# Performance work log

Measured on AMD Instinct MI355X. Metric: run time of the kernel, lower is better.

Reference implementation:

```python
import jax, jax.numpy as jnp
import numpy as np


def setup_inputs() -> dict:
    key = jax.random.key(0)
    ks = jax.random.split(key, 5)
    T, B, I, H = 512, 32, 1024, 1024
    # W/U are the stacked [W_i;W_f;W_c;W_o] and [U_i;U_f;U_c;U_o] gate weights (i,f,c,o order)
    x = jax.random.normal(ks[0], (T, B, I), dtype=jnp.float32)
    W = jax.random.normal(ks[1], (4 * H, I), dtype=jnp.float32) * (1.0 / np.sqrt(I))
    U = jax.random.normal(ks[2], (4 * H, H), dtype=jnp.float32) * (1.0 / np.sqrt(H))
    bias_ih = jax.random.normal(ks[3], (4 * H,), dtype=jnp.float32) * 0.1
    bias_hh = jax.random.normal(ks[4], (4 * H,), dtype=jnp.float32) * 0.1
    return {"x": x, "W": W, "U": U, "bias_ih": bias_ih, "bias_hh": bias_hh}


def reference(x, W, U, bias_ih, bias_hh):
    # RecurrentDropoutLSTMCell with dropout=0 (masks == 1.0), unidirectional, 1 layer.
    T, B, I = x.shape
    H = U.shape[1]
    # Precompute all input-side gate projections in one big GEMM: [T,B,4H]
    xg = jnp.einsum('tbi,gi->tbg', x, W) + (bias_ih + bias_hh)

    def step(carry, xg_t):
        h, c = carry
        g = xg_t + h @ U.T  # [B,4H]
        i_t = jax.nn.sigmoid(g[:, :H])
        f_t = jax.nn.sigmoid(g[:, H:2 * H])
        c_hat = jnp.tanh(g[:, 2 * H:3 * H])
        o_t = jax.nn.sigmoid(g[:, 3 * H:])
        c_t = f_t * c + i_t * c_hat
        h_t = o_t * jnp.tanh(c_t)
        return (h_t, c_t), h_t

    h0 = jnp.zeros((B, H), dtype=x.dtype)
    c0 = jnp.zeros((B, H), dtype=x.dtype)
    (h_n, c_n), output = jax.lax.scan(step, (h0, c0), xg)
    # matches torch module: output [T,B,H], next_hidden = (h_n,c_n) each [1,B,H]
    return output, h_n[None], c_n[None]
```

## Files before the change

### kernel.cpp

```cpp
#include <hip/hip_runtime.h>
#include <hip/hip_bf16.h>
#include <cstdint>
#include <cstddef>

#define TSTEPS 512
#define BATCH  32
#define HDIM   1024
#define GDIM   4096
#define NBLK   64

typedef __attribute__((ext_vector_type(8))) short short8;
typedef __attribute__((ext_vector_type(4))) float f32x4;

__device__ __forceinline__ unsigned short f2bf(float f) {
  uint32_t u = __float_as_uint(f);
  uint32_t r = (u + 0x7FFFu + ((u >> 16) & 1u)) >> 16;
  return (unsigned short)r;
}

__device__ __forceinline__ void async_ld16(const void* gptr, void* ldsptr) {
  __builtin_amdgcn_global_load_lds(
      (const __attribute__((address_space(1))) void*)gptr,
      (__attribute__((address_space(3))) void*)ldsptr, 16, 0, 0);
}

__global__ void cvt_bf16(const float* __restrict__ s, unsigned short* __restrict__ d, int n4) {
  int i = blockIdx.x * blockDim.x + threadIdx.x;
  if (i < n4) {
    float4 v = ((const float4*)s)[i];
    ushort4 o;
    o.x = f2bf(v.x); o.y = f2bf(v.y); o.z = f2bf(v.z); o.w = f2bf(v.w);
    ((ushort4*)d)[i] = o;
  }
}

__global__ void reorder_U(const float* __restrict__ U, unsigned short* __restrict__ Ur) {
  int i = blockIdx.x * blockDim.x + threadIdx.x;
  if (i >= GDIM * (HDIM / 4)) return;
  int k4 = i & 255;
  int row_o = i >> 8;
  int blk = row_o >> 6;
  int rem = row_o & 63;
  int g = rem >> 4;
  int jj = rem & 15;
  int src_row = g * HDIM + blk * 16 + jj;
  float4 v = ((const float4*)(U + (size_t)src_row * HDIM))[k4];
  ushort4 o;
  o.x = f2bf(v.x); o.y = f2bf(v.y); o.z = f2bf(v.z); o.w = f2bf(v.w);
  ((ushort4*)(Ur + (size_t)row_o * HDIM))[k4] = o;
}

__global__ void __launch_bounds__(256) gemm_xg(
    const unsigned short* __restrict__ A, const unsigned short* __restrict__ Bw,
    const float* __restrict__ bias_ih, const float* __restrict__ bias_hh,
    float* __restrict__ C) {
  __shared__ unsigned short As[128 * 32];
  __shared__ unsigned short Bs[128 * 32];
  const int tid = threadIdx.x;
  const int lane = tid & 63;
  const int wave = tid >> 6;
  const int m0 = blockIdx.x * 128;
  const int n0 = blockIdx.y * 128;
  const int wy = wave >> 1, wx = wave & 1;

  f32x4 acc[4][4] = {};
  const int srow = lane >> 2;
  const int skoff = (lane & 3) * 8;

  for (int k0 = 0; k0 < 1024; k0 += 32) {
    for (int s = 0; s < 2; ++s) {
      int ch = wave * 2 + s;
      int row = ch * 16 + srow;
      async_ld16(A + (size_t)(m0 + row) * 1024 + k0 + skoff, (char*)As + ch * 1024);
      async_ld16(Bw + (size_t)(n0 + row) * 1024 + k0 + skoff, (char*)Bs + ch * 1024);
    }
    __syncthreads();

    const int fr = lane & 15;
    const int fo = (lane >> 4) * 8;
    short8 a[4], b[4];
#pragma unroll
    for (int i = 0; i < 4; ++i)
      a[i] = *(const short8*)(As + (wy * 64 + i * 16 + fr) * 32 + fo);
#pragma unroll
    for (int j = 0; j < 4; ++j)
      b[j] = *(const short8*)(Bs + (wx * 64 + j * 16 + fr) * 32 + fo);
#pragma unroll
    for (int i = 0; i < 4; ++i)
#pragma unroll
      for (int j = 0; j < 4; ++j)
        acc[i][j] = __builtin_amdgcn_mfma_f32_16x16x32_bf16(a[i], b[j], acc[i][j], 0, 0, 0);
    __syncthreads();
  }

  const int fr = lane & 15;
  const int rq = (lane >> 4) * 4;
#pragma unroll
  for (int j = 0; j < 4; ++j) {
    int n = n0 + wx * 64 + j * 16 + fr;
    float bsum = bias_ih[n] + bias_hh[n];
#pragma unroll
    for (int i = 0; i < 4; ++i) {
      int mbase = m0 + wy * 64 + i * 16 + rq;
#pragma unroll
      for (int rr = 0; rr < 4; ++rr)
        C[(size_t)(mbase + rr) * GDIM + n] = acc[i][j][rr] + bsum;
    }
  }
}

__global__ void init_state(unsigned short* __restrict__ h0, float* __restrict__ c0,
                           unsigned int* __restrict__ flags) {
  int i = blockIdx.x * blockDim.x + threadIdx.x;
  if (i < 2 * BATCH * HDIM) h0[i] = 0;
  if (i < BATCH * HDIM) c0[i] = 0.f;
  if (i < NBLK * 32) flags[i] = 0;
}

__global__ void __launch_bounds__(256, 1) lstm_persist(
    const float* __restrict__ xg,
    const unsigned short* __restrict__ Urp,
    unsigned short* __restrict__ hbuf,
    float* __restrict__ cbuf,
    float* __restrict__ out,
    unsigned int* __restrict__ flags,
    int t0, int Tc) {
  __shared__ float partials[4][64][33];
  __shared__ float ex[32][17];
  const int tid = threadIdx.x;
  const int lane = tid & 63;
  const int wave = tid >> 6;
  const int blk = blockIdx.x;

  short8 Af[4][8];
  {
    const int ar = lane & 15;
    const int ak = (lane >> 4) * 8;
#pragma unroll
    for (int mt = 0; mt < 4; ++mt) {
      const unsigned short* base =
          Urp + (size_t)(blk * 64 + mt * 16 + ar) * 1024 + wave * 256 + ak;
#pragma unroll
      for (int s = 0; s < 8; ++s) Af[mt][s] = *(const short8*)(base + s * 32);
    }
  }

  const int b = tid & 31;
  const int jjb = tid >> 5;
  float creg0 = cbuf[b * 1024 + blk * 16 + jjb];
  float creg1 = cbuf[b * 1024 + blk * 16 + jjb + 8];

  float xgv[8];
  auto ld_xg = [&](int tl) {
    const float* p = xg + ((size_t)tl * 32 + b) * GDIM + blk * 16 + jjb;
#pragma unroll
    for (int g = 0; g < 4; ++g) {
      xgv[g * 2 + 0] = p[g * 1024];
      xgv[g * 2 + 1] = p[g * 1024 + 8];
    }
  };
  ld_xg(0);

  for (int tl = 0; tl < Tc; ++tl) {
    const int t = t0 + tl;
    const unsigned short* hprev = hbuf + (size_t)(t & 1) * (BATCH * HDIM);
    unsigned short* hnext = hbuf + (size_t)((t + 1) & 1) * (BATCH * HDIM);

    short8 Bf[2][8];
    {
      const int kb = wave * 256 + (lane >> 4) * 8;
#pragma unroll
      for (int nt = 0; nt < 2; ++nt) {
        const unsigned short* hb = hprev + (size_t)(nt * 16 + (lane & 15)) * 1024 + kb;
#pragma unroll
        for (int s = 0; s < 8; ++s) Bf[nt][s] = *(const short8*)(hb + s * 32);
      }
    }

    f32x4 acc[4][2] = {};
#pragma unroll
    for (int s = 0; s < 8; ++s)
#pragma unroll
      for (int mt = 0; mt < 4; ++mt)
#pragma unroll
        for (int nt = 0; nt < 2; ++nt)
          acc[mt][nt] =
              __builtin_amdgcn_mfma_f32_16x16x32_bf16(Af[mt][s], Bf[nt][s], acc[mt][nt], 0, 0, 0);

    {
      const int q4 = (lane >> 4) * 4;
      const int cc = lane & 15;
#pragma unroll
      for (int mt = 0; mt < 4; ++mt)
#pragma unroll
        for (int nt = 0; nt < 2; ++nt)
#pragma unroll
          for (int r = 0; r < 4; ++r)
            partials[wave][mt * 16 + q4 + r][nt * 16 + cc] = acc[mt][nt][r];
    }
    __syncthreads();

    float hv0, hv1;
#pragma unroll
    for (int h2 = 0; h2 < 2; ++h2) {
      const int jj = jjb + 8 * h2;
      float g[4];
#pragma unroll
      for (int gate = 0; gate < 4; ++gate) {
        const int row = gate * 16 + jj;
        g[gate] = partials[0][row][b] + partials[1][row][b] + partials[2][row][b] +
                  partials[3][row][b] + xgv[gate * 2 + h2];
      }
      float it = 1.f / (1.f + __expf(-g[0]));
      float ft = 1.f / (1.f + __expf(-g[1]));
      float ch = tanhf(g[2]);
      float ot = 1.f / (1.f + __expf(-g[3]));
      float& cr = h2 ? creg1 : creg0;
      cr = ft * cr + it * ch;
      float hvv = ot * tanhf(cr);
      if (h2) hv1 = hvv; else hv0 = hvv;
    }
    ex[b][jjb] = hv0;
    ex[b][jjb + 8] = hv1;
    __syncthreads();

    const int b2 = tid >> 3;
    const int pr = tid & 7;
    const float v0 = ex[b2][pr * 2];
    const float v1 = ex[b2][pr * 2 + 1];
    const size_t off = (size_t)b2 * 1024 + blk * 16 + pr * 2;
    {
      unsigned int pk = (unsigned)f2bf(v0) | ((unsigned)f2bf(v1) << 16);
      __hip_atomic_store((unsigned int*)(hnext + off), pk, __ATOMIC_RELAXED,
                         __HIP_MEMORY_SCOPE_AGENT);
    }

    const bool not_last = (tl + 1 < Tc);

    if (not_last) {
      asm volatile("s_waitcnt vmcnt(0)" ::: "memory");
      __syncthreads();
      if (tid == 0)
        __hip_atomic_store(&flags[blk * 32], (unsigned)(t + 1), __ATOMIC_RELAXED,
                           __HIP_MEMORY_SCOPE_AGENT);
    }

    {
      *(float2*)(out + (size_t)t * (BATCH * HDIM) + off) = make_float2(v0, v1);
      if (t == TSTEPS - 1)
        *(float2*)(out + (size_t)TSTEPS * (BATCH * HDIM) + off) = make_float2(v0, v1);
    }

    if (not_last) {
      ld_xg(tl + 1);
      if (wave == 0) {
        while (__hip_atomic_load(&flags[lane * 32], __ATOMIC_RELAXED,
                                 __HIP_MEMORY_SCOPE_AGENT) < (unsigned)(t + 1)) {
        }
        __builtin_amdgcn_fence(__ATOMIC_ACQUIRE, "agent");
      }
      __syncthreads();
    }
  }

  cbuf[b * 1024 + blk * 16 + jjb] = creg0;
  cbuf[b * 1024 + blk * 16 + jjb + 8] = creg1;
  if (t0 + Tc == TSTEPS) {
    float* cn = out + (size_t)TSTEPS * (BATCH * HDIM) + (BATCH * HDIM);
    cn[b * 1024 + blk * 16 + jjb] = creg0;
    cn[b * 1024 + blk * 16 + jjb + 8] = creg1;
  }
}

extern "C" void kernel_launch(void* const* d_in, const int* in_sizes, int n_in,
                              void* d_out, int out_size, void* d_ws, size_t ws_size,
                              hipStream_t stream) {
  const float* x = (const float*)d_in[0];
  const float* W = (const float*)d_in[1];
  const float* U = (const float*)d_in[2];
  const float* b_ih = (const float*)d_in[3];
  const float* b_hh = (const float*)d_in[4];
  float* out = (float*)d_out;

  char* ws = (char*)d_ws;
  const size_t MB8 = (size_t)8 << 20;
  unsigned short* Wb = (unsigned short*)ws;
  unsigned short* Urp = (unsigned short*)(ws + MB8);
  unsigned short* hbuf = (unsigned short*)(ws + 2 * MB8);
  float* cbuf = (float*)(ws + 2 * MB8 + 131072);
  unsigned int* flags = (unsigned int*)(ws + 2 * MB8 + 262144);
  char* chunkbase = ws + 2 * MB8 + 262144 + 16384;

  const size_t fixed_bytes = 2 * MB8 + 262144 + 16384;
  const size_t per_t = (size_t)BATCH * GDIM * 4 + (size_t)BATCH * HDIM * 2;
  int Tc = TSTEPS;
  while (Tc > 8 && fixed_bytes + (size_t)Tc * per_t > ws_size) Tc >>= 1;

  unsigned short* xb = (unsigned short*)chunkbase;
  float* xg = (float*)(chunkbase + (size_t)Tc * BATCH * HDIM * 2);

  cvt_bf16<<<4096, 256, 0, stream>>>(W, Wb, GDIM * HDIM / 4);
  reorder_U<<<4096, 256, 0, stream>>>(U, Urp);
  init_state<<<256, 256, 0, stream>>>(hbuf, cbuf, flags);

  for (int c0 = 0; c0 < TSTEPS; c0 += Tc) {
    const int Mc = Tc * BATCH;
    cvt_bf16<<<(Mc * HDIM / 4 + 255) / 256, 256, 0, stream>>>(
        x + (size_t)c0 * BATCH * HDIM, xb, Mc * HDIM / 4);
    gemm_xg<<<dim3(Mc / 128, GDIM / 128), 256, 0, stream>>>(xb, Wb, b_ih, b_hh, xg);

    const float* xg_arg = xg;
    const unsigned short* urp_arg = Urp;
    unsigned short* hbuf_arg = hbuf;
    float* cbuf_arg = cbuf;
    float* out_arg = out;
    unsigned int* flags_arg = flags;
    int t0_arg = c0, tc_arg = Tc;
    void* args[] = {&xg_arg, &urp_arg, &hbuf_arg, &cbuf_arg,
                    &out_arg, &flags_arg, &t0_arg, &tc_arg};
    hipLaunchCooperativeKernel((void*)lstm_persist, dim3(NBLK), dim3(256), args, 0, stream);
  }
}
```

Baseline: 3.121 ms.

## Split each LSTM timestep into two batch halves with finer-grained cross-block flags

The persistent LSTM kernel now processes each timestep as two 16-batch halves, each with its own MFMA pass, gate epilogue, h store and flag post. Blocks wait per half-step, so a block can begin the second half's matmul while others are still finishing theirs. This pipelines across the grid barrier instead of serializing a full 32-batch step. It doubles the number of flag waits and syncthreads per step and adds a spin-limit break that could silently continue without synchronization if exceeded.

```diff
diff --git a/kernel.cpp b/kernel.cpp
--- a/kernel.cpp
+++ b/kernel.cpp
@@ -8,6 +8,7 @@
 #define HDIM   1024
 #define GDIM   4096
 #define NBLK   64
+#define SPIN_LIMIT (1u << 22)
 
 typedef __attribute__((ext_vector_type(8))) short short8;
 typedef __attribute__((ext_vector_type(4))) float f32x4;
@@ -125,8 +126,8 @@
     float* __restrict__ out,
     unsigned int* __restrict__ flags,
     int t0, int Tc) {
-  __shared__ float partials[4][64][33];
-  __shared__ float ex[32][17];
+  __shared__ float partials[4][64][17];
+  __shared__ float ex[16][17];
   const int tid = threadIdx.x;
   const int lane = tid & 63;
   const int wave = tid >> 6;
@@ -145,130 +146,126 @@
     }
   }
 
-  const int b = tid & 31;
-  const int jjb = tid >> 5;
-  float creg0 = cbuf[b * 1024 + blk * 16 + jjb];
-  float creg1 = cbuf[b * 1024 + blk * 16 + jjb + 8];
-
-  float xgv[8];
-  auto ld_xg = [&](int tl) {
-    const float* p = xg + ((size_t)tl * 32 + b) * GDIM + blk * 16 + jjb;
-#pragma unroll
-    for (int g = 0; g < 4; ++g) {
-      xgv[g * 2 + 0] = p[g * 1024];
-      xgv[g * 2 + 1] = p[g * 1024 + 8];
-    }
+  const int b_loc = tid & 15;
+  const int jj = tid >> 4;
+  float creg[2];
+  creg[0] = cbuf[(b_loc) * 1024 + blk * 16 + jj];
+  creg[1] = cbuf[(16 + b_loc) * 1024 + blk * 16 + jj];
+
+  float xgv[4];
+  auto ld_xg = [&](int tl_, int hb_) {
+    const float* p = xg + ((size_t)tl_ * 32 + hb_ * 16 + b_loc) * GDIM + blk * 16 + jj;
+#pragma unroll
+    for (int g = 0; g < 4; ++g) xgv[g] = p[g * 1024];
   };
-  ld_xg(0);
+  ld_xg(0, 0);
 
   for (int tl = 0; tl < Tc; ++tl) {
-    const int t = t0 + tl;
-    const unsigned short* hprev = hbuf + (size_t)(t & 1) * (BATCH * HDIM);
-    unsigned short* hnext = hbuf + (size_t)((t + 1) & 1) * (BATCH * HDIM);
-
-    short8 Bf[2][8];
-    {
-      const int kb = wave * 256 + (lane >> 4) * 8;
-#pragma unroll
-      for (int nt = 0; nt < 2; ++nt) {
-        const unsigned short* hb = hprev + (size_t)(nt * 16 + (lane & 15)) * 1024 + kb;
-#pragma unroll
-        for (int s = 0; s < 8; ++s) Bf[nt][s] = *(const short8*)(hb + s * 32);
-      }
-    }
-
-    f32x4 acc[4][2] = {};
-#pragma unroll
-    for (int s = 0; s < 8; ++s)
-#pragma unroll
-      for (int mt = 0; mt < 4; ++mt)
-#pragma unroll
-        for (int nt = 0; nt < 2; ++nt)
-          acc[mt][nt] =
-              __builtin_amdgcn_mfma_f32_16x16x32_bf16(Af[mt][s], Bf[nt][s], acc[mt][nt], 0, 0, 0);
-
-    {
-      const int q4 = (lane >> 4) * 4;
-      const int cc = lane & 15;
-#pragma unroll
-      for (int mt = 0; mt < 4; ++mt)
-#pragma unroll
-        for (int nt = 0; nt < 2; ++nt)
+#pragma unroll
+    for (int hb = 0; hb < 2; ++hb) {
+      const int t = t0 + tl;
+      const unsigned short* hprev = hbuf + (size_t)(t & 1) * (BATCH * HDIM);
+      unsigned short* hnext = hbuf + (size_t)((t + 1) & 1) * (BATCH * HDIM);
+
+      if (tl > 0) {
+        if (wave == 0) {
+          const unsigned target = (unsigned)(2 * t + hb - 1);
+          unsigned spins = 0;
+          while (__hip_atomic_load(&flags[lane * 32], __ATOMIC_RELAXED,
+                                   __HIP_MEMORY_SCOPE_AGENT) < target) {
+            if (++spins > SPIN_LIMIT) break;
+          }
+          __builtin_amdgcn_fence(__ATOMIC_ACQUIRE, "agent");
+        }
+        __syncthreads();
+      }
+
+      short8 Bf[8];
+      {
+        const int kb = wave * 256 + (lane >> 4) * 8;
+        const unsigned short* hbp =
+            hprev + (size_t)(hb * 16 + (lane & 15)) * 1024 + kb;
+#pragma unroll
+        for (int s = 0; s < 8; ++s) Bf[s] = *(const short8*)(hbp + s * 32);
+      }
+
+      f32x4 acc[4] = {};
+#pragma unroll
+      for (int s = 0; s < 8; ++s)
+#pragma unroll
+        for (int mt = 0; mt < 4; ++mt)
+          acc[mt] = __builtin_amdgcn_mfma_f32_16x16x32_bf16(Af[mt][s], Bf[s], acc[mt], 0, 0, 0);
+
+      {
+        const int q4 = (lane >> 4) * 4;
+        const int cc = lane & 15;
+#pragma unroll
+        for (int mt = 0; mt < 4; ++mt)
 #pragma unroll
           for (int r = 0; r < 4; ++r)
-            partials[wave][mt * 16 + q4 + r][nt * 16 + cc] = acc[mt][nt][r];
-    }
-    __syncthreads();
-
-    float hv0, hv1;
-#pragma unroll
-    for (int h2 = 0; h2 < 2; ++h2) {
-      const int jj = jjb + 8 * h2;
+            partials[wave][mt * 16 + q4 + r][cc] = acc[mt][r];
+      }
+      __syncthreads();
+
       float g[4];
 #pragma unroll
       for (int gate = 0; gate < 4; ++gate) {
         const int row = gate * 16 + jj;
-        g[gate] = partials[0][row][b] + partials[1][row][b] + partials[2][row][b] +
-                  partials[3][row][b] + xgv[gate * 2 + h2];
+        g[gate] = partials[0][row][b_loc] + partials[1][row][b_loc] +
+                  partials[2][row][b_loc] + partials[3][row][b_loc] + xgv[gate];
       }
       float it = 1.f / (1.f + __expf(-g[0]));
       float ft = 1.f / (1.f + __expf(-g[1]));
       float ch = tanhf(g[2]);
       float ot = 1.f / (1.f + __expf(-g[3]));
-      float& cr = h2 ? creg1 : creg0;
-      cr = ft * cr + it * ch;
-      float hvv = ot * tanhf(cr);
-      if (h2) hv1 = hvv; else hv0 = hvv;
+      creg[hb] = ft * creg[hb] + it * ch;
+      const float hv = ot * tanhf(creg[hb]);
+      ex[b_loc][jj] = hv;
+      __syncthreads();
+
+      const bool storer = (tid < 128);
+      float v0 = 0.f, v1 = 0.f;
+      size_t off = 0;
+      if (storer) {
+        const int b2 = tid >> 3;
+        const int pr = tid & 7;
+        v0 = ex[b2][pr * 2];
+        v1 = ex[b2][pr * 2 + 1];
+        off = (size_t)(hb * 16 + b2) * 1024 + blk * 16 + pr * 2;
+        unsigned int pk = (unsigned)f2bf(v0) | ((unsigned)f2bf(v1) << 16);
+        __hip_atomic_store((unsigned int*)(hnext + off), pk, __ATOMIC_RELAXED,
+                           __HIP_MEMORY_SCOPE_AGENT);
+      }
+
+      const bool do_post = (tl + 1 < Tc);
+      if (do_post) {
+        asm volatile("s_waitcnt vmcnt(0)" ::: "memory");
+        __syncthreads();
+        if (tid == 0)
+          __hip_atomic_store(&flags[blk * 32], (unsigned)(2 * t + hb + 1),
+                             __ATOMIC_RELAXED, __HIP_MEMORY_SCOPE_AGENT);
+      }
+
+      if (storer) {
+        *(float2*)(out + (size_t)t * (BATCH * HDIM) + off) = make_float2(v0, v1);
+        if (t == TSTEPS - 1)
+          *(float2*)(out + (size_t)TSTEPS * (BATCH * HDIM) + off) = make_float2(v0, v1);
+      }
+
+      if (hb == 0) {
+        ld_xg(tl, 1);
+      } else if (tl + 1 < Tc) {
+        ld_xg(tl + 1, 0);
+      }
     }
-    ex[b][jjb] = hv0;
-    ex[b][jjb + 8] = hv1;
-    __syncthreads();
-
-    const int b2 = tid >> 3;
-    const int pr = tid & 7;
-    const float v0 = ex[b2][pr * 2];
-    const float v1 = ex[b2][pr * 2 + 1];
-    const size_t off = (size_t)b2 * 1024 + blk * 16 + pr * 2;
-    {
-      unsigned int pk = (unsigned)f2bf(v0) | ((unsigned)f2bf(v1) << 16);
-      __hip_atomic_store((unsigned int*)(hnext + off), pk, __ATOMIC_RELAXED,
-                         __HIP_MEMORY_SCOPE_AGENT);
-    }
-
-    const bool not_last = (tl + 1 < Tc);
-
-    if (not_last) {
-      asm volatile("s_waitcnt vmcnt(0)" ::: "memory");
-      __syncthreads();
-      if (tid == 0)
-        __hip_atomic_store(&flags[blk * 32], (unsigned)(t + 1), __ATOMIC_RELAXED,
-                           __HIP_MEMORY_SCOPE_AGENT);
-    }
-
-    {
-      *(float2*)(out + (size_t)t * (BATCH * HDIM) + off) = make_float2(v0, v1);
-      if (t == TSTEPS - 1)
-        *(float2*)(out + (size_t)TSTEPS * (BATCH * HDIM) + off) = make_float2(v0, v1);
-    }
-
-    if (not_last) {
-      ld_xg(tl + 1);
-      if (wave == 0) {
-        while (__hip_atomic_load(&flags[lane * 32], __ATOMIC_RELAXED,
-                                 __HIP_MEMORY_SCOPE_AGENT) < (unsigned)(t + 1)) {
-        }
-        __builtin_amdgcn_fence(__ATOMIC_ACQUIRE, "agent");
-      }
-      __syncthreads();
-    }
-  }
-
-  cbuf[b * 1024 + blk * 16 + jjb] = creg0;
-  cbuf[b * 1024 + blk * 16 + jjb + 8] = creg1;
+  }
+
+  cbuf[(b_loc) * 1024 + blk * 16 + jj] = creg[0];
+  cbuf[(16 + b_loc) * 1024 + blk * 16 + jj] = creg[1];
   if (t0 + Tc == TSTEPS) {
     float* cn = out + (size_t)TSTEPS * (BATCH * HDIM) + (BATCH * HDIM);
-    cn[b * 1024 + blk * 16 + jjb] = creg0;
-    cn[b * 1024 + blk * 16 + jjb + 8] = creg1;
+    cn[(b_loc) * 1024 + blk * 16 + jj] = creg[0];
+    cn[(16 + b_loc) * 1024 + blk * 16 + jj] = creg[1];
   }
 }
 
```

After: 4.101 ms. 1.31x slower.
